# Kernel tuning notes

Measured on AMD Instinct MI355X. Metric: run time of the kernel, lower is better.

## Reference

```python
import jax, jax.numpy as jnp
import numpy as np

T, B, I, H = 1024, 128, 256, 512


def setup_inputs() -> dict:
    key = jax.random.key(0)
    k1, k2, k3 = jax.random.split(key, 3)
    x = jax.random.normal(k1, (T, B, I), dtype=jnp.float32)
    # nn.Linear default init ~ U(-1/sqrt(fan_in), 1/sqrt(fan_in)); use scaled normal for stability
    Wi = jax.random.normal(k2, (H, I), dtype=jnp.float32) / np.sqrt(I)
    Wh = jax.random.normal(k3, (H, H), dtype=jnp.float32) / np.sqrt(H)
    return {"x": x, "Wi": Wi, "Wh": Wh}


def reference(x, Wi, Wh):
    # Precompute input projection for all timesteps as one batched GEMM: [T,B,H]
    xw = jnp.einsum("tbi,hi->tbh", x, Wi)
    h0 = jnp.zeros((x.shape[1], Wh.shape[0]), dtype=x.dtype)

    def step(h, xw_t):
        h_new = jnp.tanh(xw_t + h @ Wh.T)
        return h_new, h_new

    h_final, output = jax.lax.scan(step, h0, xw)
    return output, h_final
```

## Files before the change

kernel.cpp:

```cpp
#include <hip/hip_runtime.h>

#define T_STEPS 1024
#define BATCH   128
#define IDIM    256
#define HDIM    512
#define BH      (BATCH * HDIM)
#define TBH     (T_STEPS * BH)

using short8  = __attribute__((ext_vector_type(8))) short;
using floatx4 = __attribute__((ext_vector_type(4))) float;

__device__ __forceinline__ unsigned short f2bf(float f) {
  unsigned u = __builtin_bit_cast(unsigned, f);
  u += 0x7FFFu + ((u >> 16) & 1u);
  return (unsigned short)(u >> 16);
}
__device__ __forceinline__ float bf2f(unsigned short h) {
  unsigned u = ((unsigned)h) << 16;
  return __builtin_bit_cast(float, u);
}
__device__ __forceinline__ float fast_tanh(float x) {
  float e = __expf(2.0f * x);
  return 1.0f - 2.0f * __builtin_amdgcn_rcpf(e + 1.0f);
}

__device__ __forceinline__ void stage16(const float4* __restrict__ p,
                                        unsigned short* dhi, unsigned short* dlo) {
  short8 h0{}, h1{}, l0{}, l1{};
#pragma unroll
  for (int v = 0; v < 4; v++) {
    float4 fv = p[v];
    float fs[4] = {fv.x, fv.y, fv.z, fv.w};
#pragma unroll
    for (int e = 0; e < 4; e++) {
      int idx = v * 4 + e;
      unsigned short hh = f2bf(fs[e]);
      unsigned short ll = f2bf(fs[e] - bf2f(hh));
      if (idx < 8) { h0[idx] = (short)hh; l0[idx] = (short)ll; }
      else         { h1[idx - 8] = (short)hh; l1[idx - 8] = (short)ll; }
    }
  }
  *(short8*)(dhi)     = h0;
  *(short8*)(dhi + 8) = h1;
  *(short8*)(dlo)     = l0;
  *(short8*)(dlo + 8) = l1;
}

__global__ __launch_bounds__(256, 2) void xw_gemm(const float* __restrict__ x,
                                                  const float* __restrict__ Wi,
                                                  float* __restrict__ out) {
  __shared__ unsigned short Ahi[128 * 40], Alo[128 * 40];
  __shared__ unsigned short Bhi[128 * 40], Blo[128 * 40];
  const int bx   = blockIdx.x;
  const int m0   = (bx >> 2) * 128;
  const int n0   = (bx & 3) * 128;
  const int tid  = threadIdx.x;
  const int lane = tid & 63;
  const int wave = tid >> 6;
  const int q    = lane >> 4;
  const int ml   = lane & 15;
  const int wm   = (wave >> 1) * 64;
  const int wn   = (wave & 1) * 64;
  const int srow = tid & 127;
  const int skh  = tid >> 7;

  floatx4 acc[4][4];
#pragma unroll
  for (int i = 0; i < 4; i++)
#pragma unroll
    for (int j = 0; j < 4; j++)
      acc[i][j] = floatx4{0.f, 0.f, 0.f, 0.f};

  for (int kb = 0; kb < 8; kb++) {
    stage16((const float4*)(x  + (size_t)(m0 + srow) * IDIM + kb * 32 + skh * 16),
            &Ahi[srow * 40 + skh * 16], &Alo[srow * 40 + skh * 16]);
    stage16((const float4*)(Wi + (size_t)(n0 + srow) * IDIM + kb * 32 + skh * 16),
            &Bhi[srow * 40 + skh * 16], &Blo[srow * 40 + skh * 16]);
    __syncthreads();

    short8 ah[4], al[4], bh[4], bl[4];
#pragma unroll
    for (int f = 0; f < 4; f++) {
      ah[f] = *(const short8*)&Ahi[(wm + f * 16 + ml) * 40 + q * 8];
      al[f] = *(const short8*)&Alo[(wm + f * 16 + ml) * 40 + q * 8];
      bh[f] = *(const short8*)&Bhi[(wn + f * 16 + ml) * 40 + q * 8];
      bl[f] = *(const short8*)&Blo[(wn + f * 16 + ml) * 40 + q * 8];
    }
#pragma unroll
    for (int mf = 0; mf < 4; mf++)
#pragma unroll
      for (int nf = 0; nf < 4; nf++) {
        acc[mf][nf] = __builtin_amdgcn_mfma_f32_16x16x32_bf16(ah[mf], bh[nf], acc[mf][nf], 0, 0, 0);
        acc[mf][nf] = __builtin_amdgcn_mfma_f32_16x16x32_bf16(ah[mf], bl[nf], acc[mf][nf], 0, 0, 0);
        acc[mf][nf] = __builtin_amdgcn_mfma_f32_16x16x32_bf16(al[mf], bh[nf], acc[mf][nf], 0, 0, 0);
      }
    __syncthreads();
  }

#pragma unroll
  for (int mf = 0; mf < 4; mf++)
#pragma unroll
    for (int nf = 0; nf < 4; nf++)
#pragma unroll
      for (int r = 0; r < 4; r++)
        out[(size_t)(m0 + wm + mf * 16 + q * 4 + r) * HDIM + (n0 + wn + nf * 16 + ml)] =
            acc[mf][nf][r];
}

__global__ __launch_bounds__(512, 2) void rnn_scan(const float* __restrict__ Wh,
                                                   float* out,
                                                   unsigned* __restrict__ flags) {
  __shared__ unsigned short Hhi[16 * 520], Hlo[16 * 520];
  const int bg     = blockIdx.x & 7;
  const int jg     = blockIdx.x >> 3;
  const int b_base = bg * 16;
  const int j_base = jg * 128;
  const int tid    = threadIdx.x;
  const int lane   = tid & 63;
  const int wave   = tid >> 6;
  const int q      = lane >> 4;
  const int ml     = lane & 15;
  const int col    = j_base + wave * 16 + ml;
  const int rowq   = b_base + q * 4;
  const int lrow   = q * 4;

  short8 bfh[16], bfl[16];
#pragma unroll
  for (int c = 0; c < 16; c++) {
    const float4* p = (const float4*)(Wh + (size_t)col * HDIM + c * 32 + q * 8);
    float4 u = p[0], v = p[1];
    float fs[8] = {u.x, u.y, u.z, u.w, v.x, v.y, v.z, v.w};
    short8 h{}, l{};
#pragma unroll
    for (int e = 0; e < 8; e++) {
      unsigned short hh = f2bf(fs[e]);
      h[e] = (short)hh;
      l[e] = (short)f2bf(fs[e] - bf2f(hh));
    }
    bfh[c] = h;
    bfl[c] = l;
  }

  unsigned* const myflags = flags + bg * T_STEPS;

  {
    float hv[4];
#pragma unroll
    for (int r = 0; r < 4; r++) {
      size_t idx = (size_t)(rowq + r) * HDIM + col;
      hv[r] = fast_tanh(out[idx]);
      __hip_atomic_store(&out[idx], hv[r], __ATOMIC_RELAXED, __HIP_MEMORY_SCOPE_AGENT);
    }
#pragma unroll
    for (int r = 0; r < 4; r++) {
      unsigned short hh = f2bf(hv[r]);
      Hhi[(lrow + r) * 520 + col] = hh;
      Hlo[(lrow + r) * 520 + col] = f2bf(hv[r] - bf2f(hh));
    }
    __syncthreads();
    if (tid == 0)
      __hip_atomic_fetch_add(&myflags[0], 1u,
                             __ATOMIC_RELEASE, __HIP_MEMORY_SCOPE_AGENT);
  }

  for (int t = 1; t < T_STEPS; t++) {
    float* ot         = out + (size_t)t * BH;
    const float* otm1 = out + (size_t)(t - 1) * BH;

    float xwv[4];
#pragma unroll
    for (int r = 0; r < 4; r++) xwv[r] = ot[(size_t)(rowq + r) * HDIM + col];

    if (tid == 0) {
      int k = 0;
      for (;;) {
        unsigned v = __hip_atomic_load(&myflags[t - 1],
                                       __ATOMIC_RELAXED, __HIP_MEMORY_SCOPE_AGENT);
        if (v >= 4u) break;
        if ((k++ & 3) == 3) {
          v = __hip_atomic_load(&myflags[t - 1],
                                __ATOMIC_ACQUIRE, __HIP_MEMORY_SCOPE_AGENT);
          if (v >= 4u) break;
        }
        __builtin_amdgcn_s_sleep(1);
      }
      __builtin_amdgcn_fence(__ATOMIC_ACQUIRE, "agent");
    }
    __syncthreads();

    if (tid < 384) {
      const int s   = tid >> 7;
      const int pc  = ((jg + 1 + s) & 3) * 128;
      const int row = (tid >> 3) & 15;
      const int k0  = (tid & 7) * 16;
      stage16((const float4*)(otm1 + (size_t)(b_base + row) * HDIM + pc + k0),
              &Hhi[row * 520 + pc + k0], &Hlo[row * 520 + pc + k0]);
    }
    __syncthreads();

    floatx4 acc = {xwv[0], xwv[1], xwv[2], xwv[3]};
#pragma unroll
    for (int c = 0; c < 16; c++) {
      short8 ahi = *(const short8*)&Hhi[ml * 520 + c * 32 + q * 8];
      short8 alo = *(const short8*)&Hlo[ml * 520 + c * 32 + q * 8];
      acc = __builtin_amdgcn_mfma_f32_16x16x32_bf16(ahi, bfh[c], acc, 0, 0, 0);
      acc = __builtin_amdgcn_mfma_f32_16x16x32_bf16(ahi, bfl[c], acc, 0, 0, 0);
      acc = __builtin_amdgcn_mfma_f32_16x16x32_bf16(alo, bfh[c], acc, 0, 0, 0);
    }

    float hv[4];
#pragma unroll
    for (int r = 0; r < 4; r++) {
      hv[r] = fast_tanh(acc[r]);
      __hip_atomic_store(&ot[(size_t)(rowq + r) * HDIM + col], hv[r],
                         __ATOMIC_RELAXED, __HIP_MEMORY_SCOPE_AGENT);
      if (t == T_STEPS - 1)
        out[(size_t)TBH + (size_t)(rowq + r) * HDIM + col] = hv[r];
    }
    __syncthreads();
    if (tid == 0)
      __hip_atomic_fetch_add(&myflags[t], 1u,
                             __ATOMIC_RELEASE, __HIP_MEMORY_SCOPE_AGENT);

#pragma unroll
    for (int r = 0; r < 4; r++) {
      unsigned short hh = f2bf(hv[r]);
      Hhi[(lrow + r) * 520 + col] = hh;
      Hlo[(lrow + r) * 520 + col] = f2bf(hv[r] - bf2f(hh));
    }
  }
}

extern "C" void kernel_launch(void* const* d_in, const int* in_sizes, int n_in,
                              void* d_out, int out_size, void* d_ws, size_t ws_size,
                              hipStream_t stream) {
  const float* x  = (const float*)d_in[0];
  const float* Wi = (const float*)d_in[1];
  const float* Wh = (const float*)d_in[2];
  float* out      = (float*)d_out;
  unsigned* flags = (unsigned*)d_ws;

  hipMemsetAsync(d_ws, 0, 8 * T_STEPS * sizeof(unsigned), stream);

  xw_gemm<<<dim3((131072 / 128) * (HDIM / 128)), dim3(256), 0, stream>>>(x, Wi, out);

  rnn_scan<<<dim3(32), dim3(512), 0, stream>>>(Wh, out, flags);
}
```

Measured before the change: 3.728 ms.

## Overlap own-chunk recurrent MFMAs with the cross-block flag wait

Reorders each block's Wh fragments so its own 128-column slice of h_{t-1}, already in LDS, is multiplied before spinning on the inter-block flag. Only the other three slices are consumed after the wait. It also prefetches the next step's xw values during the current step and changes spin polling to relaxed system-scope loads with a rarer acquire reload. An extra barrier at the end of each step keeps the early own-slice reads from racing with the LDS writes of the new h, which adds some synchronization cost per step.

```diff
diff --git a/kernel.cpp b/kernel.cpp
--- a/kernel.cpp
+++ b/kernel.cpp
@@ -123,10 +123,12 @@
   const int col    = j_base + wave * 16 + ml;
   const int rowq   = b_base + q * 4;
   const int lrow   = q * 4;
+  const int cown   = jg * 4;
 
   short8 bfh[16], bfl[16];
 #pragma unroll
-  for (int c = 0; c < 16; c++) {
+  for (int s = 0; s < 16; s++) {
+    const int c = (cown + s) & 15;
     const float4* p = (const float4*)(Wh + (size_t)col * HDIM + c * 32 + q * 8);
     float4 u = p[0], v = p[1];
     float fs[8] = {u.x, u.y, u.z, u.w, v.x, v.y, v.z, v.w};
@@ -137,11 +139,12 @@
       h[e] = (short)hh;
       l[e] = (short)f2bf(fs[e] - bf2f(hh));
     }
-    bfh[c] = h;
-    bfl[c] = l;
+    bfh[s] = h;
+    bfl[s] = l;
   }
 
   unsigned* const myflags = flags + bg * T_STEPS;
+  float xwv[4];
 
   {
     float hv[4];
@@ -157,6 +160,8 @@
       Hhi[(lrow + r) * 520 + col] = hh;
       Hlo[(lrow + r) * 520 + col] = f2bf(hv[r] - bf2f(hh));
     }
+#pragma unroll
+    for (int r = 0; r < 4; r++) xwv[r] = out[(size_t)BH + (size_t)(rowq + r) * HDIM + col];
     __syncthreads();
     if (tid == 0)
       __hip_atomic_fetch_add(&myflags[0], 1u,
@@ -164,20 +169,27 @@
   }
 
   for (int t = 1; t < T_STEPS; t++) {
-    float* ot         = out + (size_t)t * BH;
+    float* ot = out + (size_t)t * BH;
     const float* otm1 = out + (size_t)(t - 1) * BH;
 
-    float xwv[4];
-#pragma unroll
-    for (int r = 0; r < 4; r++) xwv[r] = ot[(size_t)(rowq + r) * HDIM + col];
+    floatx4 acc = {xwv[0], xwv[1], xwv[2], xwv[3]};
+#pragma unroll
+    for (int s = 0; s < 4; s++) {
+      const int c = (cown + s) & 15;
+      short8 ahi = *(const short8*)&Hhi[ml * 520 + c * 32 + q * 8];
+      short8 alo = *(const short8*)&Hlo[ml * 520 + c * 32 + q * 8];
+      acc = __builtin_amdgcn_mfma_f32_16x16x32_bf16(ahi, bfh[s], acc, 0, 0, 0);
+      acc = __builtin_amdgcn_mfma_f32_16x16x32_bf16(ahi, bfl[s], acc, 0, 0, 0);
+      acc = __builtin_amdgcn_mfma_f32_16x16x32_bf16(alo, bfh[s], acc, 0, 0, 0);
+    }
 
     if (tid == 0) {
       int k = 0;
       for (;;) {
         unsigned v = __hip_atomic_load(&myflags[t - 1],
-                                       __ATOMIC_RELAXED, __HIP_MEMORY_SCOPE_AGENT);
+                                       __ATOMIC_RELAXED, __HIP_MEMORY_SCOPE_SYSTEM);
         if (v >= 4u) break;
-        if ((k++ & 3) == 3) {
+        if ((++k & 255) == 0) {
           v = __hip_atomic_load(&myflags[t - 1],
                                 __ATOMIC_ACQUIRE, __HIP_MEMORY_SCOPE_AGENT);
           if (v >= 4u) break;
@@ -198,14 +210,14 @@
     }
     __syncthreads();
 
-    floatx4 acc = {xwv[0], xwv[1], xwv[2], xwv[3]};
-#pragma unroll
-    for (int c = 0; c < 16; c++) {
+#pragma unroll
+    for (int s = 4; s < 16; s++) {
+      const int c = (cown + s) & 15;
       short8 ahi = *(const short8*)&Hhi[ml * 520 + c * 32 + q * 8];
       short8 alo = *(const short8*)&Hlo[ml * 520 + c * 32 + q * 8];
-      acc = __builtin_amdgcn_mfma_f32_16x16x32_bf16(ahi, bfh[c], acc, 0, 0, 0);
-      acc = __builtin_amdgcn_mfma_f32_16x16x32_bf16(ahi, bfl[c], acc, 0, 0, 0);
-      acc = __builtin_amdgcn_mfma_f32_16x16x32_bf16(alo, bfh[c], acc, 0, 0, 0);
+      acc = __builtin_amdgcn_mfma_f32_16x16x32_bf16(ahi, bfh[s], acc, 0, 0, 0);
+      acc = __builtin_amdgcn_mfma_f32_16x16x32_bf16(ahi, bfl[s], acc, 0, 0, 0);
+      acc = __builtin_amdgcn_mfma_f32_16x16x32_bf16(alo, bfh[s], acc, 0, 0, 0);
     }
 
     float hv[4];
@@ -217,6 +229,13 @@
       if (t == T_STEPS - 1)
         out[(size_t)TBH + (size_t)(rowq + r) * HDIM + col] = hv[r];
     }
+
+    if (t + 1 < T_STEPS) {
+#pragma unroll
+      for (int r = 0; r < 4; r++)
+        xwv[r] = out[(size_t)(t + 1) * BH + (size_t)(rowq + r) * HDIM + col];
+    }
+
     __syncthreads();
     if (tid == 0)
       __hip_atomic_fetch_add(&myflags[t], 1u,
@@ -228,6 +247,7 @@
       Hhi[(lrow + r) * 520 + col] = hh;
       Hlo[(lrow + r) * 520 + col] = f2bf(hv[r] - bf2f(hh));
     }
+    __syncthreads();
   }
 }
 
```

After: 4.281 ms. +14.8%, slower.
